# Kernel optimization log

Hardware: AMD Instinct MI355X
Metric: run time of the kernel (lower is better)

## Reference

```python
import jax, jax.numpy as jnp
import numpy as np

BATCH = 256
VOCAB = 50000
NUM_TOPICS = 50
TIME_SLICES = 10
EMBED_DIM = 1024


def setup_inputs() -> dict:
    key = jax.random.key(0)
    k1, k2, k3, k4 = jax.random.split(key, 4)
    theta = jax.random.uniform(k1, (BATCH, NUM_TOPICS), dtype=jnp.float32)
    theta = theta / jnp.sum(theta, axis=-1, keepdims=True)  # topic distribution
    word_embeddings = jax.random.normal(k2, (VOCAB, EMBED_DIM), dtype=jnp.float32)
    topic_embeddings = jax.random.normal(k3, (TIME_SLICES, NUM_TOPICS, EMBED_DIM), dtype=jnp.float32)
    time_index = jax.random.randint(k4, (BATCH,), 0, TIME_SLICES, dtype=jnp.int64)
    return {"theta": theta, "word_embeddings": word_embeddings,
            "topic_embeddings": topic_embeddings, "time_index": time_index}


def reference(theta, word_embeddings, topic_embeddings, time_index):
    # beta_t = softmax(topic_embeddings[t] @ W^T) over vocab, for all time slices: (T, K, V)
    logits = jnp.einsum('tke,ve->tkv', topic_embeddings, word_embeddings)
    betas = jax.nn.softmax(logits, axis=-1)
    # word_dist[i] = theta[i] @ betas[time_index[i]]. Compute for all t then gather
    # (avoids materializing a (B, K, V) gathered tensor).
    all_out = jnp.einsum('bk,tkv->btv', theta, betas)  # (B, T, V)
    out = jnp.take_along_axis(all_out, time_index[:, None, None], axis=1)[:, 0, :]
    return out  # (B, V)
```

## Files before the change

### kernel.cpp

```cpp
#include <hip/hip_runtime.h>
#include <hip/hip_bf16.h>


typedef __bf16 bf16_t;
typedef __bf16 bf16x4 __attribute__((ext_vector_type(4)));
typedef __bf16 bf16x8 __attribute__((ext_vector_type(8)));
typedef float f32x4 __attribute__((ext_vector_type(4)));

typedef __attribute__((address_space(1))) void gvoid;
typedef __attribute__((address_space(3))) void svoid;
#define GLDS(SRC, DST) \
    __builtin_amdgcn_global_load_lds((gvoid*)(SRC), (svoid*)(DST), 16, 0, 0)
#define MFMA16(A, B, C) __builtin_amdgcn_mfma_f32_16x16x32_bf16((A), (B), (C), 0, 0, 0)

#define SHIFT 180.0f
#define TTS2 72

__device__ __forceinline__ void cvt8(float4 a, float4 b, bf16x8& h, bf16x8& l)
{
    float f[8] = {a.x, a.y, a.z, a.w, b.x, b.y, b.z, b.w};
#pragma unroll
    for (int j = 0; j < 8; ++j) {
        bf16_t hh = (bf16_t)f[j];
        h[j] = hh;
        l[j] = (bf16_t)(f[j] - (float)hh);
    }
}

__global__ void prep(const float* __restrict__ x, bf16_t* __restrict__ hi,
                     bf16_t* __restrict__ lo, float* __restrict__ rsum)
{
    int i = blockIdx.x * 256 + threadIdx.x;
    if (i < 512) rsum[i] = 0.f;
    if (i < 512000) {
        float v = x[i];
        bf16_t h = (bf16_t)v;
        hi[i] = h;
        lo[i] = (bf16_t)(v - (float)h);
    }
}

__global__ __launch_bounds__(256, 2)
void gemm_logits(const bf16_t* __restrict__ Ahi, const bf16_t* __restrict__ Alo,
                 const float* __restrict__ W, bf16_t* __restrict__ Pt,
                 float* __restrict__ Rsum)
{
    __shared__ __align__(16) bf16_t sm[32768];
    bf16_t* AsH = sm;
    bf16_t* AsL = sm + 8192;
    bf16_t* BsH = sm + 16384;
    bf16_t* BsL = sm + 24576;

    const int tid = threadIdx.x;
    const int wv = tid >> 6, lane = tid & 63;
    const int wm = wv >> 1, wn = wv & 1;

    const int lin = blockIdx.x;
    const int xcd = lin & 7, wi = lin >> 3;
    const int nid = (xcd < 4 ? xcd * 196 : 784 + (xcd - 4) * 195) + wi;
    const int bm0 = (nid & 3) * 128;
    const int bn0 = (nid >> 2) * 128;

    const int lrow = lane & 15, q = lane >> 4;
    const int srow = lane >> 3, sgrp = (lane & 7) ^ srow;

    const int wrow_l = tid >> 1;
    int wrow_g = bn0 + wrow_l; if (wrow_g > 49999) wrow_g = 49999;
    const int kq = tid & 1;
    const float4* wp = (const float4*)(W + (long)wrow_g * 1024) + kq * 8;
    int so[4];
#pragma unroll
    for (int jj = 0; jj < 4; ++jj)
        so[jj] = wrow_l * 64 + (((kq * 4 + jj) ^ (wrow_l & 7)) * 8);

    f32x4 acc[4][4] = {};
    float4 wcur[8], wnxt[8];
#pragma unroll
    for (int j = 0; j < 8; ++j) wcur[j] = wp[j];

    for (int t = 0; t < 16; ++t) {
        const int k0 = t * 64;
#pragma unroll
        for (int cc = 0; cc < 4; ++cc) {
            const int ch = wv * 4 + cc;
            int ar = bm0 + ch * 8 + srow; if (ar > 499) ar = 499;
            GLDS(Ahi + (long)ar * 1024 + k0 + sgrp * 8, AsH + ch * 512);
            GLDS(Alo + (long)ar * 1024 + k0 + sgrp * 8, AsL + ch * 512);
        }
#pragma unroll
        for (int jj = 0; jj < 4; ++jj) {
            bf16x8 h, l;
            cvt8(wcur[2 * jj], wcur[2 * jj + 1], h, l);
            *(bf16x8*)(BsH + so[jj]) = h;
            *(bf16x8*)(BsL + so[jj]) = l;
        }
        __syncthreads();
        if (t < 15) {
            const int o = (t + 1) * 16;
#pragma unroll
            for (int j = 0; j < 8; ++j) wnxt[j] = wp[o + j];
        }
#pragma unroll
        for (int kk = 0; kk < 2; ++kk) {
            const int kg = kk * 4 + q;
            bf16x8 ah[4], al[4], bh[4], bl[4];
#pragma unroll
            for (int a = 0; a < 4; ++a) {
                const int row = wm * 64 + a * 16 + lrow;
                const int off = row * 64 + ((kg ^ (row & 7)) * 8);
                ah[a] = *(const bf16x8*)(AsH + off);
                al[a] = *(const bf16x8*)(AsL + off);
            }
#pragma unroll
            for (int b = 0; b < 4; ++b) {
                const int n = wn * 64 + b * 16 + lrow;
                const int off = n * 64 + ((kg ^ (n & 7)) * 8);
                bh[b] = *(const bf16x8*)(BsH + off);
                bl[b] = *(const bf16x8*)(BsL + off);
            }
            __builtin_amdgcn_s_setprio(1);
#pragma unroll
            for (int a = 0; a < 4; ++a)
#pragma unroll
                for (int b = 0; b < 4; ++b) {
                    acc[a][b] = MFMA16(ah[a], bh[b], acc[a][b]);
                    acc[a][b] = MFMA16(ah[a], bl[b], acc[a][b]);
                    acc[a][b] = MFMA16(al[a], bh[b], acc[a][b]);
                }
            __builtin_amdgcn_s_setprio(0);
        }
        __syncthreads();
        if (t < 15) {
#pragma unroll
            for (int j = 0; j < 8; ++j) wcur[j] = wnxt[j];
        }
    }

#pragma unroll
    for (int a = 0; a < 4; ++a) {
        float rs[4] = {0.f, 0.f, 0.f, 0.f};
#pragma unroll
        for (int b = 0; b < 4; ++b) {
            const bool cok = (bn0 + wn * 64 + b * 16 + lrow) < 50000;
#pragma unroll
            for (int r = 0; r < 4; ++r) {
                const float e = __expf(acc[a][b][r] - SHIFT);
                acc[a][b][r] = e;
                if (cok) rs[r] += e;
            }
        }
#pragma unroll
        for (int r = 0; r < 4; ++r) {
            float v = rs[r];
            v += __shfl_xor(v, 1, 16);
            v += __shfl_xor(v, 2, 16);
            v += __shfl_xor(v, 4, 16);
            v += __shfl_xor(v, 8, 16);
            const int row = bm0 + wm * 64 + a * 16 + q * 4 + r;
            if (lrow == 0 && row < 500) atomicAdd(Rsum + row, v);
        }
    }
    bf16_t* Tt = sm + wv * (64 * TTS2);
#pragma unroll
    for (int a = 0; a < 4; ++a)
#pragma unroll
        for (int b = 0; b < 4; ++b) {
            bf16x4 p;
#pragma unroll
            for (int r = 0; r < 4; ++r) p[r] = (bf16_t)acc[a][b][r];
            *(bf16x4*)(Tt + (b * 16 + lrow) * TTS2 + a * 16 + q * 4) = p;
        }
    const long kbase = bm0 + wm * 64;
    const int cbase = bn0 + wn * 64;
#pragma unroll
    for (int it = 0; it < 8; ++it) {
        const int u = it * 64 + lane;
        const int vl = u >> 3, ck = u & 7;
        bf16x8 d = *(const bf16x8*)(Tt + vl * TTS2 + ck * 8);
        *(bf16x8*)(Pt + (long)(cbase + vl) * 512 + kbase + ck * 8) = d;
    }
}

__global__ void build_theta2(const float* __restrict__ theta,
                             const int* __restrict__ tidx,
                             const float* __restrict__ rsum,
                             bf16_t* __restrict__ T2)
{
    const int i = blockIdx.x, r = threadIdx.x;
    const int base = tidx[i] * 50;
    bf16_t v = (bf16_t)0.0f;
    if (r >= base && r < base + 50)
        v = (bf16_t)(theta[i * 50 + (r - base)] / rsum[r]);
    T2[i * 512 + r] = v;
}

__global__ __launch_bounds__(256, 4)
void gemm_out(const bf16_t* __restrict__ T2, const bf16_t* __restrict__ Pt,
              float* __restrict__ out)
{
    __shared__ __align__(16) bf16_t As[256 * 64];
    __shared__ __align__(16) bf16_t Bs[64 * 64];
    const int tid = threadIdx.x;
    const int wave = tid >> 6, lane = tid & 63;
    const int bn0 = blockIdx.x * 64;
    const int lrow = lane & 15, q = lane >> 4;
    const int srow = lane >> 3, sgrp = (lane & 7) ^ srow;

    f32x4 acc[4][4] = {};

    for (int k0 = 0; k0 < 512; k0 += 64) {
#pragma unroll
        for (int cc = 0; cc < 8; ++cc) {
            const int ch = wave * 8 + cc;
            GLDS(T2 + (ch * 8 + srow) * 512 + k0 + sgrp * 8, As + ch * 512);
        }
#pragma unroll
        for (int cc = 0; cc < 2; ++cc) {
            const int ch = wave * 2 + cc;
            const long brow = bn0 + ch * 8 + srow;
            GLDS(Pt + brow * 512 + k0 + sgrp * 8, Bs + ch * 512);
        }
        __syncthreads();
#pragma unroll
        for (int kk = 0; kk < 2; ++kk) {
            const int kg = kk * 4 + q;
            bf16x8 af[4], bfr[4];
#pragma unroll
            for (int a = 0; a < 4; ++a) {
                const int row = wave * 64 + a * 16 + lrow;
                af[a] = *(const bf16x8*)(As + row * 64 + ((kg ^ (row & 7)) * 8));
            }
#pragma unroll
            for (int b = 0; b < 4; ++b) {
                const int n = b * 16 + lrow;
                bfr[b] = *(const bf16x8*)(Bs + n * 64 + ((kg ^ (n & 7)) * 8));
            }
#pragma unroll
            for (int a = 0; a < 4; ++a)
#pragma unroll
                for (int b = 0; b < 4; ++b)
                    acc[a][b] = MFMA16(af[a], bfr[b], acc[a][b]);
        }
        __syncthreads();
    }
#pragma unroll
    for (int a = 0; a < 4; ++a) {
        const int row0 = wave * 64 + a * 16 + q * 4;
#pragma unroll
        for (int b = 0; b < 4; ++b) {
            const int col = bn0 + b * 16 + lrow;
            if (col < 50000) {
#pragma unroll
                for (int r = 0; r < 4; ++r)
                    out[(long)(row0 + r) * 50000 + col] = acc[a][b][r];
            }
        }
    }
}

extern "C" void kernel_launch(void* const* d_in, const int* in_sizes, int n_in,
                              void* d_out, int out_size, void* d_ws, size_t ws_size,
                              hipStream_t stream)
{
    const float* theta = (const float*)d_in[0];
    const float* wemb  = (const float*)d_in[1];
    const float* temb  = (const float*)d_in[2];
    const int*   tidx  = (const int*)d_in[3];
    float* out = (float*)d_out;

    char* ws = (char*)d_ws;
    bf16_t* Pt    = (bf16_t*)ws;
    float*  rsum  = (float*)(ws + 51249152);
    bf16_t* a_hi  = (bf16_t*)(ws + 51251200);
    bf16_t* a_lo  = (bf16_t*)(ws + 52275200);
    bf16_t* T2    = (bf16_t*)(ws + 53299200);

    prep        <<<dim3(2000), 256, 0, stream>>>(temb, a_hi, a_lo, rsum);
    gemm_logits <<<dim3(1564), 256, 0, stream>>>(a_hi, a_lo, wemb, Pt, rsum);
    build_theta2<<<dim3(256),  512, 0, stream>>>(theta, tidx, rsum, T2);
    gemm_out    <<<dim3(782),  256, 0, stream>>>(T2, Pt, out);
}
```

Baseline: 464.6 us.

## Restructure GEMMs to full-M blocks with packed A read directly from global

Result: slower. 509.0 us (+9.5%).

```diff
diff --git a/kernel.cpp b/kernel.cpp
--- a/kernel.cpp
+++ b/kernel.cpp
@@ -27,113 +27,116 @@
     }
 }
 
-__global__ void prep(const float* __restrict__ x, bf16_t* __restrict__ hi,
-                     bf16_t* __restrict__ lo, float* __restrict__ rsum)
-{
-    int i = blockIdx.x * 256 + threadIdx.x;
-    if (i < 512) rsum[i] = 0.f;
-    if (i < 512000) {
-        float v = x[i];
-        bf16_t h = (bf16_t)v;
-        hi[i] = h;
-        lo[i] = (bf16_t)(v - (float)h);
-    }
-}
-
-__global__ __launch_bounds__(256, 2)
-void gemm_logits(const bf16_t* __restrict__ Ahi, const bf16_t* __restrict__ Alo,
+__global__ void prep_pack(const float* __restrict__ x, bf16_t* __restrict__ hi,
+                          bf16_t* __restrict__ lo, float* __restrict__ rsum)
+{
+    const int j = blockIdx.x * 256 + threadIdx.x;
+    if (j < 512) rsum[j] = 0.f;
+    const int r = j >> 7, g = j & 127;
+    float4 v0 = {0.f, 0.f, 0.f, 0.f}, v1 = v0;
+    if (r < 500) {
+        v0 = *(const float4*)(x + r * 1024 + g * 8);
+        v1 = *(const float4*)(x + r * 1024 + g * 8 + 4);
+    }
+    bf16x8 h, l;
+    cvt8(v0, v1, h, l);
+    *(bf16x8*)(hi + g * 4096 + r * 8) = h;
+    *(bf16x8*)(lo + g * 4096 + r * 8) = l;
+}
+
+__global__ __launch_bounds__(512, 4)
+void gemm_logits(const bf16_t* __restrict__ Ahp, const bf16_t* __restrict__ Alp,
                  const float* __restrict__ W, bf16_t* __restrict__ Pt,
                  float* __restrict__ Rsum)
 {
-    __shared__ __align__(16) bf16_t sm[32768];
-    bf16_t* AsH = sm;
-    bf16_t* AsL = sm + 8192;
-    bf16_t* BsH = sm + 16384;
-    bf16_t* BsL = sm + 24576;
+    __shared__ __align__(16) bf16_t sm[36864];
+    bf16_t* BsH = sm;
+    bf16_t* BsL = sm + 4096;
 
     const int tid = threadIdx.x;
     const int wv = tid >> 6, lane = tid & 63;
-    const int wm = wv >> 1, wn = wv & 1;
-
-    const int lin = blockIdx.x;
-    const int xcd = lin & 7, wi = lin >> 3;
-    const int nid = (xcd < 4 ? xcd * 196 : 784 + (xcd - 4) * 195) + wi;
-    const int bm0 = (nid & 3) * 128;
-    const int bn0 = (nid >> 2) * 128;
-
+    const int bn0 = blockIdx.x * 64;
     const int lrow = lane & 15, q = lane >> 4;
-    const int srow = lane >> 3, sgrp = (lane & 7) ^ srow;
-
-    const int wrow_l = tid >> 1;
+
+    const int wrow_l = tid >> 3;
     int wrow_g = bn0 + wrow_l; if (wrow_g > 49999) wrow_g = 49999;
-    const int kq = tid & 1;
-    const float4* wp = (const float4*)(W + (long)wrow_g * 1024) + kq * 8;
-    int so[4];
-#pragma unroll
-    for (int jj = 0; jj < 4; ++jj)
-        so[jj] = wrow_l * 64 + (((kq * 4 + jj) ^ (wrow_l & 7)) * 8);
+    const int kch = tid & 7;
+    const float4* wp0 = (const float4*)(W + (long)wrow_g * 1024) + kch * 2;
+    const int sob = wrow_l * 64 + ((kch ^ (wrow_l & 7)) * 8);
+
+    const int arow = wv * 64 + lrow;
 
     f32x4 acc[4][4] = {};
-    float4 wcur[8], wnxt[8];
-#pragma unroll
-    for (int j = 0; j < 8; ++j) wcur[j] = wp[j];
+    float4 wc0 = wp0[0], wc1 = wp0[1];
+    float4 wn0, wn1;
 
     for (int t = 0; t < 16; ++t) {
-        const int k0 = t * 64;
-#pragma unroll
-        for (int cc = 0; cc < 4; ++cc) {
-            const int ch = wv * 4 + cc;
-            int ar = bm0 + ch * 8 + srow; if (ar > 499) ar = 499;
-            GLDS(Ahi + (long)ar * 1024 + k0 + sgrp * 8, AsH + ch * 512);
-            GLDS(Alo + (long)ar * 1024 + k0 + sgrp * 8, AsL + ch * 512);
-        }
-#pragma unroll
-        for (int jj = 0; jj < 4; ++jj) {
+        if (t < 15) { wn0 = wp0[(t + 1) * 16]; wn1 = wp0[(t + 1) * 16 + 1]; }
+        bf16x8 ah0[4], al0[4];
+        {
+            const int g = t * 8 + q;
+#pragma unroll
+            for (int a = 0; a < 4; ++a) {
+                const int ro = g * 4096 + (arow + a * 16) * 8;
+                ah0[a] = *(const bf16x8*)(Ahp + ro);
+                al0[a] = *(const bf16x8*)(Alp + ro);
+            }
+        }
+        {
             bf16x8 h, l;
-            cvt8(wcur[2 * jj], wcur[2 * jj + 1], h, l);
-            *(bf16x8*)(BsH + so[jj]) = h;
-            *(bf16x8*)(BsL + so[jj]) = l;
-        }
-        __syncthreads();
-        if (t < 15) {
-            const int o = (t + 1) * 16;
-#pragma unroll
-            for (int j = 0; j < 8; ++j) wnxt[j] = wp[o + j];
-        }
-#pragma unroll
-        for (int kk = 0; kk < 2; ++kk) {
-            const int kg = kk * 4 + q;
-            bf16x8 ah[4], al[4], bh[4], bl[4];
+            cvt8(wc0, wc1, h, l);
+            *(bf16x8*)(BsH + sob) = h;
+            *(bf16x8*)(BsL + sob) = l;
+        }
+        asm volatile("s_waitcnt lgkmcnt(0)" ::: "memory");
+        __builtin_amdgcn_s_barrier();
+        {
+            const int kg = q;
+#pragma unroll
+            for (int b = 0; b < 4; ++b) {
+                const int n = b * 16 + lrow;
+                const int off = n * 64 + ((kg ^ (n & 7)) * 8);
+                bf16x8 bh = *(const bf16x8*)(BsH + off);
+                bf16x8 bl = *(const bf16x8*)(BsL + off);
+                __builtin_amdgcn_s_setprio(1);
+#pragma unroll
+                for (int a = 0; a < 4; ++a) {
+                    acc[a][b] = MFMA16(ah0[a], bh, acc[a][b]);
+                    acc[a][b] = MFMA16(ah0[a], bl, acc[a][b]);
+                    acc[a][b] = MFMA16(al0[a], bh, acc[a][b]);
+                }
+                __builtin_amdgcn_s_setprio(0);
+            }
+        }
+        {
+            const int g = t * 8 + 4 + q;
+            bf16x8 ah[4], al[4];
 #pragma unroll
             for (int a = 0; a < 4; ++a) {
-                const int row = wm * 64 + a * 16 + lrow;
-                const int off = row * 64 + ((kg ^ (row & 7)) * 8);
-                ah[a] = *(const bf16x8*)(AsH + off);
-                al[a] = *(const bf16x8*)(AsL + off);
-            }
+                const int ro = g * 4096 + (arow + a * 16) * 8;
+                ah[a] = *(const bf16x8*)(Ahp + ro);
+                al[a] = *(const bf16x8*)(Alp + ro);
+            }
+            const int kg = 4 + q;
 #pragma unroll
             for (int b = 0; b < 4; ++b) {
-                const int n = wn * 64 + b * 16 + lrow;
+                const int n = b * 16 + lrow;
                 const int off = n * 64 + ((kg ^ (n & 7)) * 8);
-                bh[b] = *(const bf16x8*)(BsH + off);
-                bl[b] = *(const bf16x8*)(BsL + off);
-            }
-            __builtin_amdgcn_s_setprio(1);
-#pragma unroll
-            for (int a = 0; a < 4; ++a)
-#pragma unroll
-                for (int b = 0; b < 4; ++b) {
-                    acc[a][b] = MFMA16(ah[a], bh[b], acc[a][b]);
-                    acc[a][b] = MFMA16(ah[a], bl[b], acc[a][b]);
-                    acc[a][b] = MFMA16(al[a], bh[b], acc[a][b]);
+                bf16x8 bh = *(const bf16x8*)(BsH + off);
+                bf16x8 bl = *(const bf16x8*)(BsL + off);
+                __builtin_amdgcn_s_setprio(1);
+#pragma unroll
+                for (int a = 0; a < 4; ++a) {
+                    acc[a][b] = MFMA16(ah[a], bh, acc[a][b]);
+                    acc[a][b] = MFMA16(ah[a], bl, acc[a][b]);
+                    acc[a][b] = MFMA16(al[a], bh, acc[a][b]);
                 }
-            __builtin_amdgcn_s_setprio(0);
-        }
-        __syncthreads();
-        if (t < 15) {
-#pragma unroll
-            for (int j = 0; j < 8; ++j) wcur[j] = wnxt[j];
-        }
+                __builtin_amdgcn_s_setprio(0);
+            }
+        }
+        asm volatile("s_waitcnt lgkmcnt(0)" ::: "memory");
+        __builtin_amdgcn_s_barrier();
+        wc0 = wn0; wc1 = wn1;
     }
 
 #pragma unroll
@@ -141,7 +144,7 @@
         float rs[4] = {0.f, 0.f, 0.f, 0.f};
 #pragma unroll
         for (int b = 0; b < 4; ++b) {
-            const bool cok = (bn0 + wn * 64 + b * 16 + lrow) < 50000;
+            const bool cok = (bn0 + b * 16 + lrow) < 50000;
 #pragma unroll
             for (int r = 0; r < 4; ++r) {
                 const float e = __expf(acc[a][b][r] - SHIFT);
@@ -156,7 +159,7 @@
             v += __shfl_xor(v, 2, 16);
             v += __shfl_xor(v, 4, 16);
             v += __shfl_xor(v, 8, 16);
-            const int row = bm0 + wm * 64 + a * 16 + q * 4 + r;
+            const int row = wv * 64 + a * 16 + q * 4 + r;
             if (lrow == 0 && row < 500) atomicAdd(Rsum + row, v);
         }
     }
@@ -170,78 +173,67 @@
             for (int r = 0; r < 4; ++r) p[r] = (bf16_t)acc[a][b][r];
             *(bf16x4*)(Tt + (b * 16 + lrow) * TTS2 + a * 16 + q * 4) = p;
         }
-    const long kbase = bm0 + wm * 64;
-    const int cbase = bn0 + wn * 64;
+    const long kbase = wv * 64;
 #pragma unroll
     for (int it = 0; it < 8; ++it) {
         const int u = it * 64 + lane;
         const int vl = u >> 3, ck = u & 7;
         bf16x8 d = *(const bf16x8*)(Tt + vl * TTS2 + ck * 8);
-        *(bf16x8*)(Pt + (long)(cbase + vl) * 512 + kbase + ck * 8) = d;
+        *(bf16x8*)(Pt + (long)(bn0 + vl) * 512 + kbase + ck * 8) = d;
     }
 }
 
 __global__ void build_theta2(const float* __restrict__ theta,
                              const int* __restrict__ tidx,
                              const float* __restrict__ rsum,
-                             bf16_t* __restrict__ T2)
-{
-    const int i = blockIdx.x, r = threadIdx.x;
+                             bf16_t* __restrict__ T2p)
+{
+    const int i = blockIdx.x, rr = threadIdx.x;
     const int base = tidx[i] * 50;
     bf16_t v = (bf16_t)0.0f;
-    if (r >= base && r < base + 50)
-        v = (bf16_t)(theta[i * 50 + (r - base)] / rsum[r]);
-    T2[i * 512 + r] = v;
+    if (rr >= base && rr < base + 50)
+        v = (bf16_t)(theta[i * 50 + (rr - base)] / rsum[rr]);
+    T2p[(rr >> 3) * 2048 + i * 8 + (rr & 7)] = v;
 }
 
 __global__ __launch_bounds__(256, 4)
-void gemm_out(const bf16_t* __restrict__ T2, const bf16_t* __restrict__ Pt,
+void gemm_out(const bf16_t* __restrict__ T2p, const bf16_t* __restrict__ Pt,
               float* __restrict__ out)
 {
-    __shared__ __align__(16) bf16_t As[256 * 64];
-    __shared__ __align__(16) bf16_t Bs[64 * 64];
+    __shared__ __align__(16) bf16_t Bs[32768];
     const int tid = threadIdx.x;
     const int wave = tid >> 6, lane = tid & 63;
     const int bn0 = blockIdx.x * 64;
     const int lrow = lane & 15, q = lane >> 4;
-    const int srow = lane >> 3, sgrp = (lane & 7) ^ srow;
+
+#pragma unroll
+    for (int rr = 0; rr < 16; ++rr) {
+        const int ub = rr * 4096 + wave * 1024;
+        const int off = ub + lane * 16;
+        const int row = off >> 10;
+        const int c = (off >> 4) & 63;
+        const int cs = c ^ (row & 7);
+        GLDS(Pt + (long)(bn0 + row) * 512 + cs * 8, ((char*)Bs) + ub);
+    }
+    __syncthreads();
 
     f32x4 acc[4][4] = {};
-
-    for (int k0 = 0; k0 < 512; k0 += 64) {
-#pragma unroll
-        for (int cc = 0; cc < 8; ++cc) {
-            const int ch = wave * 8 + cc;
-            GLDS(T2 + (ch * 8 + srow) * 512 + k0 + sgrp * 8, As + ch * 512);
-        }
-#pragma unroll
-        for (int cc = 0; cc < 2; ++cc) {
-            const int ch = wave * 2 + cc;
-            const long brow = bn0 + ch * 8 + srow;
-            GLDS(Pt + brow * 512 + k0 + sgrp * 8, Bs + ch * 512);
-        }
-        __syncthreads();
-#pragma unroll
-        for (int kk = 0; kk < 2; ++kk) {
-            const int kg = kk * 4 + q;
-            bf16x8 af[4], bfr[4];
-#pragma unroll
-            for (int a = 0; a < 4; ++a) {
-                const int row = wave * 64 + a * 16 + lrow;
-                af[a] = *(const bf16x8*)(As + row * 64 + ((kg ^ (row & 7)) * 8));
-            }
-#pragma unroll
-            for (int b = 0; b < 4; ++b) {
-                const int n = b * 16 + lrow;
-                bfr[b] = *(const bf16x8*)(Bs + n * 64 + ((kg ^ (n & 7)) * 8));
-            }
+#pragma unroll 4
+    for (int kk = 0; kk < 16; ++kk) {
+        const int g = kk * 4 + q;
+        bf16x8 af[4];
+#pragma unroll
+        for (int a = 0; a < 4; ++a)
+            af[a] = *(const bf16x8*)(T2p + g * 2048 +
+                                     (wave * 64 + a * 16 + lrow) * 8);
+#pragma unroll
+        for (int b = 0; b < 4; ++b) {
+            const int n = b * 16 + lrow;
+            bf16x8 bfr = *(const bf16x8*)(Bs + n * 512 + ((g ^ (n & 7)) * 8));
 #pragma unroll
             for (int a = 0; a < 4; ++a)
-#pragma unroll
-                for (int b = 0; b < 4; ++b)
-                    acc[a][b] = MFMA16(af[a], bfr[b], acc[a][b]);
-        }
-        __syncthreads();
+                acc[a][b] = MFMA16(af[a], bfr, acc[a][b]);
+        }
     }
 #pragma unroll
     for (int a = 0; a < 4; ++a) {
@@ -269,14 +261,14 @@
     float* out = (float*)d_out;
 
     char* ws = (char*)d_ws;
-    bf16_t* Pt    = (bf16_t*)ws;
-    float*  rsum  = (float*)(ws + 51249152);
-    bf16_t* a_hi  = (bf16_t*)(ws + 51251200);
-    bf16_t* a_lo  = (bf16_t*)(ws + 52275200);
-    bf16_t* T2    = (bf16_t*)(ws + 53299200);
-
-    prep        <<<dim3(2000), 256, 0, stream>>>(temb, a_hi, a_lo, rsum);
-    gemm_logits <<<dim3(1564), 256, 0, stream>>>(a_hi, a_lo, wemb, Pt, rsum);
-    build_theta2<<<dim3(256),  512, 0, stream>>>(theta, tidx, rsum, T2);
-    gemm_out    <<<dim3(782),  256, 0, stream>>>(T2, Pt, out);
-}
+    bf16_t* Pt   = (bf16_t*)ws;
+    float*  rsum = (float*)(ws + 51249152);
+    bf16_t* Ahp  = (bf16_t*)(ws + 51251200);
+    bf16_t* Alp  = (bf16_t*)(ws + 52299776);
+    bf16_t* T2p  = (bf16_t*)(ws + 51251200);
+
+    prep_pack   <<<dim3(256), 256, 0, stream>>>(temb, Ahp, Alp, rsum);
+    gemm_logits <<<dim3(782), 512, 0, stream>>>(Ahp, Alp, wemb, Pt, rsum);
+    build_theta2<<<dim3(256), 512, 0, stream>>>(theta, tidx, rsum, T2p);
+    gemm_out    <<<dim3(782), 256, 0, stream>>>(T2p, Pt, out);
+}
```
